# Performance work log

Measured on AMD Instinct MI355X. Metric: run time of the kernel, lower is better.

Reference implementation:

```python
import jax, jax.numpy as jnp
import numpy as np

MARGIN = 0.3
N, D = 8192, 128
NUM_CLASSES = 512


def setup_inputs() -> dict:
    key = jax.random.key(0)
    k1, k2 = jax.random.split(key)
    embeddings = jax.random.normal(k1, (N, D), dtype=jnp.float32)
    targets = jax.random.randint(k2, (N,), 0, NUM_CLASSES, dtype=jnp.int64)
    return {"embeddings": embeddings, "targets": targets}


def reference(embeddings, targets):
    x = embeddings.astype(jnp.float32)
    # pairwise squared-euclidean: ||xi||^2 + ||xj||^2 - 2 xi.xj, clamped then sqrt
    sq = jnp.sum(x * x, axis=1)  # [N]
    dist = sq[:, None] + sq[None, :] - 2.0 * (x @ x.T)
    dist = jnp.sqrt(jnp.clip(dist, 1e-12, None))  # [N, N]

    is_pos = targets[:, None] == targets[None, :]  # includes diagonal, as in torch code

    # batch-hard mining: per-row hardest positive (max) and hardest negative (min)
    dist_ap = jnp.max(jnp.where(is_pos, dist, -jnp.inf), axis=1)
    dist_an = jnp.min(jnp.where(is_pos, jnp.inf, dist), axis=1)

    # MarginRankingLoss(margin)(dist_an, dist_ap, y=1) = mean(relu(margin - (dist_an - dist_ap)))
    loss = jnp.mean(jax.nn.relu(dist_ap - dist_an + MARGIN))
    return loss
```

## Files before the change

kernel.cpp:

```cpp
#include <hip/hip_runtime.h>
#include <hip/hip_bf16.h>

#define N_ROWS 8192
#define DIM 128
#define MARGIN_F 0.3f

typedef __attribute__((ext_vector_type(8))) short short8;
typedef __attribute__((ext_vector_type(4))) float f32x4;
typedef __attribute__((ext_vector_type(4))) int int4v;

__global__ __launch_bounds__(256) void prep_kernel(
    const float* __restrict__ x, const int* __restrict__ tgt,
    unsigned short* __restrict__ xbA, unsigned short* __restrict__ xbB,
    float2* __restrict__ meta, int* __restrict__ apb, int* __restrict__ anb) {
  const int w = threadIdx.x >> 6, l = threadIdx.x & 63;
  const int row = blockIdx.x * 4 + w;
  float2 v = reinterpret_cast<const float2*>(x + (size_t)row * DIM)[l];
  __hip_bfloat16 b0 = __float2bfloat16(v.x);
  __hip_bfloat16 b1 = __float2bfloat16(v.y);
  __hip_bfloat16 a0 = __float2bfloat16(-2.f * v.x);
  __hip_bfloat16 a1 = __float2bfloat16(-2.f * v.y);
  ushort2 stB, stA;
  stB.x = *reinterpret_cast<unsigned short*>(&b0);
  stB.y = *reinterpret_cast<unsigned short*>(&b1);
  stA.x = *reinterpret_cast<unsigned short*>(&a0);
  stA.y = *reinterpret_cast<unsigned short*>(&a1);
  const int c16 = row >> 4, l15r = row & 15;
  const int unit = c16 * 256 + (l >> 4) * 64 + ((l >> 2) & 3) * 16 + l15r;
  reinterpret_cast<ushort2*>(xbB)[unit * 4 + (l & 3)] = stB;
  reinterpret_cast<ushort2*>(xbA)[unit * 4 + (l & 3)] = stA;

  float s = v.x * v.x + v.y * v.y;
  #pragma unroll
  for (int off = 32; off >= 1; off >>= 1) s += __shfl_xor(s, off);
  if (l == 0) {
    float2 m;
    m.x = s;
    m.y = __int_as_float(tgt[row]);
    meta[row] = m;
    apb[row] = 0x00000000;
    anb[row] = 0x7f800000;
  }
}

__global__ __launch_bounds__(256, 2) void gram_mine_kernel(
    const unsigned short* __restrict__ xbA, const unsigned short* __restrict__ xbB,
    const float2* __restrict__ meta, int* __restrict__ apb, int* __restrict__ anb) {
  const int t = threadIdx.x;
  const int w = t >> 6, l = t & 63;
  const int l15 = l & 15, l4 = l >> 4;
  const int rb = blockIdx.x * 128 + w * 32;
  const int chunk = blockIdx.y * 512;
  const int chunkb = chunk >> 4;

  const short8* xfA = reinterpret_cast<const short8*>(xbA);
  const short8* xfB = reinterpret_cast<const short8*>(xbB);

  short8 a0[4], a1[4];
  #pragma unroll
  for (int kk = 0; kk < 4; ++kk) {
    a0[kk] = xfA[(rb >> 4) * 256 + kk * 64 + l];
    a1[kk] = xfA[((rb >> 4) + 1) * 256 + kk * 64 + l];
  }

  int t_r[8];
  #pragma unroll
  for (int rf = 0; rf < 2; ++rf)
    #pragma unroll
    for (int rg = 0; rg < 4; ++rg)
      t_r[rf * 4 + rg] = __float_as_int(meta[rb + rf * 16 + l4 * 4 + rg].y);

  float ap2[8], an2[8];
  #pragma unroll
  for (int i = 0; i < 8; ++i) { ap2[i] = -__builtin_inff(); an2[i] = __builtin_inff(); }

  short8 b0[8], b1[8], b2[8], b3[8];
  float2 m0[2], m1[2], m2[2], m3[2];
  f32x4 accA[2][2], accB[2][2];

#define PREF(IDX, BB, MC) do {                                                \
    const int cb16_ = chunkb + (IDX) * 2;                                     \
    _Pragma("unroll")                                                         \
    for (int kk_ = 0; kk_ < 4; ++kk_) {                                       \
      BB[kk_ * 2 + 0] = xfB[(cb16_ + 0) * 256 + kk_ * 64 + l];                \
      BB[kk_ * 2 + 1] = xfB[(cb16_ + 1) * 256 + kk_ * 64 + l];                \
    }                                                                         \
    MC[0] = meta[chunk + (IDX) * 32 + l15];                                   \
    MC[1] = meta[chunk + (IDX) * 32 + 16 + l15]; } while (0)

#define MFMA_T(BB, MC, ACC) do {                                              \
    _Pragma("unroll")                                                         \
    for (int cf_ = 0; cf_ < 2; ++cf_) {                                       \
      float s_ = MC[cf_].x;                                                   \
      f32x4 ci_ = {s_, s_, s_, s_};                                           \
      ACC[0][cf_] = ci_; ACC[1][cf_] = ci_;                                   \
    }                                                                         \
    __builtin_amdgcn_s_setprio(1);                                            \
    _Pragma("unroll")                                                         \
    for (int kk_ = 0; kk_ < 4; ++kk_) {                                       \
      _Pragma("unroll")                                                       \
      for (int cf_ = 0; cf_ < 2; ++cf_) {                                     \
        ACC[0][cf_] = __builtin_amdgcn_mfma_f32_16x16x32_bf16(                \
            a0[kk_], BB[kk_ * 2 + cf_], ACC[0][cf_], 0, 0, 0);                \
        ACC[1][cf_] = __builtin_amdgcn_mfma_f32_16x16x32_bf16(                \
            a1[kk_], BB[kk_ * 2 + cf_], ACC[1][cf_], 0, 0, 0);                \
      } }                                                                     \
    __builtin_amdgcn_s_setprio(0); } while (0)

#define EPI_T(ACC, MC) do {                                                   \
    _Pragma("unroll")                                                         \
    for (int cf_ = 0; cf_ < 2; ++cf_) {                                       \
      const int tc_ = __float_as_int(MC[cf_].y);                              \
      _Pragma("unroll")                                                       \
      for (int rf_ = 0; rf_ < 2; ++rf_) {                                     \
        _Pragma("unroll")                                                     \
        for (int rg_ = 0; rg_ < 4; ++rg_) {                                   \
          const int ix_ = rf_ * 4 + rg_;                                      \
          float v_ = ACC[rf_][cf_][rg_];                                      \
          bool p_ = (t_r[ix_] == tc_);                                        \
          ap2[ix_] = p_ ? fmaxf(ap2[ix_], v_) : ap2[ix_];                     \
          an2[ix_] = p_ ? an2[ix_] : fminf(an2[ix_], v_);                     \
        } } } } while (0)

  PREF(0, b0, m0);
  PREF(1, b1, m1);
  PREF(2, b2, m2); MFMA_T(b0, m0, accA);
  PREF(3, b3, m3); MFMA_T(b1, m1, accB); EPI_T(accA, m0);

  #pragma unroll 1
  for (int q = 0; q < 3; ++q) {
    const int tb = 4 * q + 2;
    PREF(tb + 2, b0, m0); MFMA_T(b2, m2, accA); EPI_T(accB, m1);
    PREF(tb + 3, b1, m1); MFMA_T(b3, m3, accB); EPI_T(accA, m2);
    PREF(tb + 4, b2, m2); MFMA_T(b0, m0, accA); EPI_T(accB, m3);
    PREF(tb + 5, b3, m3); MFMA_T(b1, m1, accB); EPI_T(accA, m0);
  }
  MFMA_T(b2, m2, accA); EPI_T(accB, m1);
  MFMA_T(b3, m3, accB); EPI_T(accA, m2);
  EPI_T(accB, m3);

#undef PREF
#undef MFMA_T
#undef EPI_T

  #pragma unroll
  for (int i = 0; i < 8; ++i) {
    #pragma unroll
    for (int off = 1; off < 16; off <<= 1) {
      ap2[i] = fmaxf(ap2[i], __shfl_xor(ap2[i], off));
      an2[i] = fminf(an2[i], __shfl_xor(an2[i], off));
    }
  }
  if (l15 == 0) {
    #pragma unroll
    for (int rf = 0; rf < 2; ++rf)
      #pragma unroll
      for (int rg = 0; rg < 4; ++rg) {
        int row = rb + rf * 16 + l4 * 4 + rg;
        float sqr = meta[row].x;
        float a2 = fmaxf(ap2[rf * 4 + rg] + sqr, 1e-12f);
        float n2 = fmaxf(an2[rf * 4 + rg] + sqr, 1e-12f);
        atomicMax(apb + row, __float_as_int(a2));
        atomicMin(anb + row, __float_as_int(n2));
      }
  }
}

__global__ __launch_bounds__(1024) void loss_kernel(
    const int4v* __restrict__ apb, const int4v* __restrict__ anb,
    float* __restrict__ out) {
  __shared__ float red[16];
  float s = 0.f;
  for (int i = threadIdx.x; i < N_ROWS / 4; i += 1024) {
    int4v a4 = apb[i], n4 = anb[i];
    #pragma unroll
    for (int j = 0; j < 4; ++j) {
      float ap = sqrtf(__int_as_float(a4[j]));
      float an = sqrtf(__int_as_float(n4[j]));
      float li = ap - an + MARGIN_F;
      s += li > 0.f ? li : 0.f;
    }
  }
  #pragma unroll
  for (int off = 32; off >= 1; off >>= 1) s += __shfl_xor(s, off);
  const int w = threadIdx.x >> 6, l = threadIdx.x & 63;
  if (l == 0) red[w] = s;
  __syncthreads();
  if (threadIdx.x < 16) {
    float v = red[threadIdx.x];
    #pragma unroll
    for (int off = 8; off >= 1; off >>= 1) v += __shfl_xor(v, off);
    if (threadIdx.x == 0) out[0] = v / (float)N_ROWS;
  }
}

extern "C" void kernel_launch(void* const* d_in, const int* in_sizes, int n_in,
                              void* d_out, int out_size, void* d_ws, size_t ws_size,
                              hipStream_t stream) {
  const float* x = (const float*)d_in[0];
  const int* tgt = (const int*)d_in[1];
  float* out = (float*)d_out;

  char* ws = (char*)d_ws;
  unsigned short* xbA = (unsigned short*)ws;
  unsigned short* xbB = (unsigned short*)(ws + 2097152);
  float2* meta = (float2*)(ws + 4194304);
  int* apb = (int*)(ws + 4194304 + 65536);
  int* anb = (int*)(ws + 4194304 + 65536 + 32768);

  prep_kernel<<<2048, 256, 0, stream>>>(x, tgt, xbA, xbB, meta, apb, anb);
  gram_mine_kernel<<<dim3(64, 16), 256, 0, stream>>>(xbA, xbB, meta, apb, anb);
  loss_kernel<<<1, 1024, 0, stream>>>((const int4v*)apb, (const int4v*)anb, out);
}
```

Measured before the change: 47.90 us.

## Double per-wave row tile to 64 rows and simplify B prefetch to double buffering

Each wave now keeps 64 rows of A fragments in registers instead of 32, so every loaded B column fragment is reused across four MFMA row tiles. This halves the number of row blocks in the grid (32x16) and the total B traffic from global/L2. The four-deep B prefetch ring with separate MFMA/epilogue stages is replaced by a two-buffer ring with the epilogue fused right after the MFMAs. Register pressure rises and the grid shrinks to 512 blocks, which may reduce occupancy and MFMA/epilogue overlap.

```diff
diff --git a/kernel.cpp b/kernel.cpp
--- a/kernel.cpp
+++ b/kernel.cpp
@@ -49,34 +49,33 @@
   const int t = threadIdx.x;
   const int w = t >> 6, l = t & 63;
   const int l15 = l & 15, l4 = l >> 4;
-  const int rb = blockIdx.x * 128 + w * 32;
+  const int rb = blockIdx.x * 256 + w * 64;
   const int chunk = blockIdx.y * 512;
   const int chunkb = chunk >> 4;
 
   const short8* xfA = reinterpret_cast<const short8*>(xbA);
   const short8* xfB = reinterpret_cast<const short8*>(xbB);
 
-  short8 a0[4], a1[4];
-  #pragma unroll
-  for (int kk = 0; kk < 4; ++kk) {
-    a0[kk] = xfA[(rb >> 4) * 256 + kk * 64 + l];
-    a1[kk] = xfA[((rb >> 4) + 1) * 256 + kk * 64 + l];
-  }
-
-  int t_r[8];
-  #pragma unroll
-  for (int rf = 0; rf < 2; ++rf)
+  short8 a[4][4];
+  #pragma unroll
+  for (int rf = 0; rf < 4; ++rf)
+    #pragma unroll
+    for (int kk = 0; kk < 4; ++kk)
+      a[rf][kk] = xfA[((rb >> 4) + rf) * 256 + kk * 64 + l];
+
+  int t_r[16];
+  #pragma unroll
+  for (int rf = 0; rf < 4; ++rf)
     #pragma unroll
     for (int rg = 0; rg < 4; ++rg)
       t_r[rf * 4 + rg] = __float_as_int(meta[rb + rf * 16 + l4 * 4 + rg].y);
 
-  float ap2[8], an2[8];
-  #pragma unroll
-  for (int i = 0; i < 8; ++i) { ap2[i] = -__builtin_inff(); an2[i] = __builtin_inff(); }
-
-  short8 b0[8], b1[8], b2[8], b3[8];
-  float2 m0[2], m1[2], m2[2], m3[2];
-  f32x4 accA[2][2], accB[2][2];
+  float ap2[16], an2[16];
+  #pragma unroll
+  for (int i = 0; i < 16; ++i) { ap2[i] = -__builtin_inff(); an2[i] = __builtin_inff(); }
+
+  short8 b0[8], b1[8];
+  float2 m0[2], m1[2];
 
 #define PREF(IDX, BB, MC) do {                                                \
     const int cb16_ = chunkb + (IDX) * 2;                                     \
@@ -88,63 +87,54 @@
     MC[0] = meta[chunk + (IDX) * 32 + l15];                                   \
     MC[1] = meta[chunk + (IDX) * 32 + 16 + l15]; } while (0)
 
-#define MFMA_T(BB, MC, ACC) do {                                              \
+#define TILE(BB, MC) do {                                                     \
+    f32x4 acc_[4][2];                                                         \
     _Pragma("unroll")                                                         \
     for (int cf_ = 0; cf_ < 2; ++cf_) {                                       \
       float s_ = MC[cf_].x;                                                   \
       f32x4 ci_ = {s_, s_, s_, s_};                                           \
-      ACC[0][cf_] = ci_; ACC[1][cf_] = ci_;                                   \
+      _Pragma("unroll")                                                       \
+      for (int rf_ = 0; rf_ < 4; ++rf_) acc_[rf_][cf_] = ci_;                 \
     }                                                                         \
     __builtin_amdgcn_s_setprio(1);                                            \
     _Pragma("unroll")                                                         \
     for (int kk_ = 0; kk_ < 4; ++kk_) {                                       \
       _Pragma("unroll")                                                       \
       for (int cf_ = 0; cf_ < 2; ++cf_) {                                     \
-        ACC[0][cf_] = __builtin_amdgcn_mfma_f32_16x16x32_bf16(                \
-            a0[kk_], BB[kk_ * 2 + cf_], ACC[0][cf_], 0, 0, 0);                \
-        ACC[1][cf_] = __builtin_amdgcn_mfma_f32_16x16x32_bf16(                \
-            a1[kk_], BB[kk_ * 2 + cf_], ACC[1][cf_], 0, 0, 0);                \
+        _Pragma("unroll")                                                     \
+        for (int rf_ = 0; rf_ < 4; ++rf_)                                     \
+          acc_[rf_][cf_] = __builtin_amdgcn_mfma_f32_16x16x32_bf16(           \
+              a[rf_][kk_], BB[kk_ * 2 + cf_], acc_[rf_][cf_], 0, 0, 0);       \
       } }                                                                     \
-    __builtin_amdgcn_s_setprio(0); } while (0)
-
-#define EPI_T(ACC, MC) do {                                                   \
+    __builtin_amdgcn_s_setprio(0);                                            \
     _Pragma("unroll")                                                         \
     for (int cf_ = 0; cf_ < 2; ++cf_) {                                       \
       const int tc_ = __float_as_int(MC[cf_].y);                              \
       _Pragma("unroll")                                                       \
-      for (int rf_ = 0; rf_ < 2; ++rf_) {                                     \
+      for (int rf_ = 0; rf_ < 4; ++rf_) {                                     \
         _Pragma("unroll")                                                     \
         for (int rg_ = 0; rg_ < 4; ++rg_) {                                   \
           const int ix_ = rf_ * 4 + rg_;                                      \
-          float v_ = ACC[rf_][cf_][rg_];                                      \
+          float v_ = acc_[rf_][cf_][rg_];                                     \
           bool p_ = (t_r[ix_] == tc_);                                        \
           ap2[ix_] = p_ ? fmaxf(ap2[ix_], v_) : ap2[ix_];                     \
           an2[ix_] = p_ ? an2[ix_] : fminf(an2[ix_], v_);                     \
         } } } } while (0)
 
   PREF(0, b0, m0);
-  PREF(1, b1, m1);
-  PREF(2, b2, m2); MFMA_T(b0, m0, accA);
-  PREF(3, b3, m3); MFMA_T(b1, m1, accB); EPI_T(accA, m0);
-
   #pragma unroll 1
-  for (int q = 0; q < 3; ++q) {
-    const int tb = 4 * q + 2;
-    PREF(tb + 2, b0, m0); MFMA_T(b2, m2, accA); EPI_T(accB, m1);
-    PREF(tb + 3, b1, m1); MFMA_T(b3, m3, accB); EPI_T(accA, m2);
-    PREF(tb + 4, b2, m2); MFMA_T(b0, m0, accA); EPI_T(accB, m3);
-    PREF(tb + 5, b3, m3); MFMA_T(b1, m1, accB); EPI_T(accA, m0);
-  }
-  MFMA_T(b2, m2, accA); EPI_T(accB, m1);
-  MFMA_T(b3, m3, accB); EPI_T(accA, m2);
-  EPI_T(accB, m3);
+  for (int q = 0; q < 7; ++q) {
+    PREF(2 * q + 1, b1, m1); TILE(b0, m0);
+    PREF(2 * q + 2, b0, m0); TILE(b1, m1);
+  }
+  PREF(15, b1, m1); TILE(b0, m0);
+  TILE(b1, m1);
 
 #undef PREF
-#undef MFMA_T
-#undef EPI_T
-
-  #pragma unroll
-  for (int i = 0; i < 8; ++i) {
+#undef TILE
+
+  #pragma unroll
+  for (int i = 0; i < 16; ++i) {
     #pragma unroll
     for (int off = 1; off < 16; off <<= 1) {
       ap2[i] = fmaxf(ap2[i], __shfl_xor(ap2[i], off));
@@ -153,7 +143,7 @@
   }
   if (l15 == 0) {
     #pragma unroll
-    for (int rf = 0; rf < 2; ++rf)
+    for (int rf = 0; rf < 4; ++rf)
       #pragma unroll
       for (int rg = 0; rg < 4; ++rg) {
         int row = rb + rf * 16 + l4 * 4 + rg;
@@ -209,6 +199,6 @@
   int* anb = (int*)(ws + 4194304 + 65536 + 32768);
 
   prep_kernel<<<2048, 256, 0, stream>>>(x, tgt, xbA, xbB, meta, apb, anb);
-  gram_mine_kernel<<<dim3(64, 16), 256, 0, stream>>>(xbA, xbB, meta, apb, anb);
+  gram_mine_kernel<<<dim3(32, 16), 256, 0, stream>>>(xbA, xbB, meta, apb, anb);
   loss_kernel<<<1, 1024, 0, stream>>>((const int4v*)apb, (const int4v*)anb, out);
 }
```

Result: faster. 45.29 us (-5.5%).

## Interleave two column streams per block and parallelize loss reduction across blocks

Applied to the files above, without the earlier changes.

The gram/mining kernel now gives each block two 512-column chunks and interleaves their MFMA and epilogue work with a shallower two-buffer prefetch. The grid's y dimension is halved, which cuts the number of atomic row merges. The single-block loss kernel is replaced by eight blocks that combine partial sums through a fixed-point 64-bit atomic and a last-block-done counter. This gives more independent MFMA chains per wave and a more parallel final reduction, at the cost of a different register footprint, fewer blocks, and a quantized loss sum.

```diff
diff --git a/kernel.cpp b/kernel.cpp
--- a/kernel.cpp
+++ b/kernel.cpp
@@ -7,12 +7,13 @@
 
 typedef __attribute__((ext_vector_type(8))) short short8;
 typedef __attribute__((ext_vector_type(4))) float f32x4;
-typedef __attribute__((ext_vector_type(4))) int int4v;
 
 __global__ __launch_bounds__(256) void prep_kernel(
     const float* __restrict__ x, const int* __restrict__ tgt,
     unsigned short* __restrict__ xbA, unsigned short* __restrict__ xbB,
-    float2* __restrict__ meta, int* __restrict__ apb, int* __restrict__ anb) {
+    float2* __restrict__ meta, int* __restrict__ apb, int* __restrict__ anb,
+    unsigned long long* __restrict__ lsum, unsigned int* __restrict__ lcnt) {
+  if (blockIdx.x == 0 && threadIdx.x == 0) { *lsum = 0ull; *lcnt = 0u; }
   const int w = threadIdx.x >> 6, l = threadIdx.x & 63;
   const int row = blockIdx.x * 4 + w;
   float2 v = reinterpret_cast<const float2*>(x + (size_t)row * DIM)[l];
@@ -50,8 +51,8 @@
   const int w = t >> 6, l = t & 63;
   const int l15 = l & 15, l4 = l >> 4;
   const int rb = blockIdx.x * 128 + w * 32;
-  const int chunk = blockIdx.y * 512;
-  const int chunkb = chunk >> 4;
+  const int cu = blockIdx.y * 1024;
+  const int cv = cu + 512;
 
   const short8* xfA = reinterpret_cast<const short8*>(xbA);
   const short8* xfB = reinterpret_cast<const short8*>(xbB);
@@ -74,19 +75,19 @@
   #pragma unroll
   for (int i = 0; i < 8; ++i) { ap2[i] = -__builtin_inff(); an2[i] = __builtin_inff(); }
 
-  short8 b0[8], b1[8], b2[8], b3[8];
-  float2 m0[2], m1[2], m2[2], m3[2];
-  f32x4 accA[2][2], accB[2][2];
-
-#define PREF(IDX, BB, MC) do {                                                \
-    const int cb16_ = chunkb + (IDX) * 2;                                     \
+  short8 bu[8], bv[8];
+  float2 mu0[2], mu1[2], mv0[2], mv1[2];
+  f32x4 accu[2][2], accv[2][2];
+
+#define PREF(BASE, IDX, BB, MC) do {                                          \
+    const int cb16_ = ((BASE) >> 4) + (IDX) * 2;                              \
     _Pragma("unroll")                                                         \
     for (int kk_ = 0; kk_ < 4; ++kk_) {                                       \
       BB[kk_ * 2 + 0] = xfB[(cb16_ + 0) * 256 + kk_ * 64 + l];                \
       BB[kk_ * 2 + 1] = xfB[(cb16_ + 1) * 256 + kk_ * 64 + l];                \
     }                                                                         \
-    MC[0] = meta[chunk + (IDX) * 32 + l15];                                   \
-    MC[1] = meta[chunk + (IDX) * 32 + 16 + l15]; } while (0)
+    MC[0] = meta[(BASE) + (IDX) * 32 + l15];                                  \
+    MC[1] = meta[(BASE) + (IDX) * 32 + 16 + l15]; } while (0)
 
 #define MFMA_T(BB, MC, ACC) do {                                              \
     _Pragma("unroll")                                                         \
@@ -122,22 +123,21 @@
           an2[ix_] = p_ ? an2[ix_] : fminf(an2[ix_], v_);                     \
         } } } } while (0)
 
-  PREF(0, b0, m0);
-  PREF(1, b1, m1);
-  PREF(2, b2, m2); MFMA_T(b0, m0, accA);
-  PREF(3, b3, m3); MFMA_T(b1, m1, accB); EPI_T(accA, m0);
+  PREF(cu, 0, bu, mu0);
+  PREF(cv, 0, bv, mv0);
 
   #pragma unroll 1
-  for (int q = 0; q < 3; ++q) {
-    const int tb = 4 * q + 2;
-    PREF(tb + 2, b0, m0); MFMA_T(b2, m2, accA); EPI_T(accB, m1);
-    PREF(tb + 3, b1, m1); MFMA_T(b3, m3, accB); EPI_T(accA, m2);
-    PREF(tb + 4, b2, m2); MFMA_T(b0, m0, accA); EPI_T(accB, m3);
-    PREF(tb + 5, b3, m3); MFMA_T(b1, m1, accB); EPI_T(accA, m0);
-  }
-  MFMA_T(b2, m2, accA); EPI_T(accB, m1);
-  MFMA_T(b3, m3, accB); EPI_T(accA, m2);
-  EPI_T(accB, m3);
+  for (int q = 0; q < 8; ++q) {
+    const int te = 2 * q;
+    const int n1 = te + 1;
+    const int n2 = (te + 2 < 16) ? te + 2 : 15;
+    MFMA_T(bu, mu0, accu); PREF(cu, n1, bu, mu1);
+    MFMA_T(bv, mv0, accv); PREF(cv, n1, bv, mv1);
+    EPI_T(accu, mu0); EPI_T(accv, mv0);
+    MFMA_T(bu, mu1, accu); PREF(cu, n2, bu, mu0);
+    MFMA_T(bv, mv1, accv); PREF(cv, n2, bv, mv0);
+    EPI_T(accu, mu1); EPI_T(accv, mv1);
+  }
 
 #undef PREF
 #undef MFMA_T
@@ -167,20 +167,15 @@
 }
 
 __global__ __launch_bounds__(1024) void loss_kernel(
-    const int4v* __restrict__ apb, const int4v* __restrict__ anb,
+    const int* __restrict__ apb, const int* __restrict__ anb,
+    unsigned long long* __restrict__ lsum, unsigned int* __restrict__ lcnt,
     float* __restrict__ out) {
   __shared__ float red[16];
-  float s = 0.f;
-  for (int i = threadIdx.x; i < N_ROWS / 4; i += 1024) {
-    int4v a4 = apb[i], n4 = anb[i];
-    #pragma unroll
-    for (int j = 0; j < 4; ++j) {
-      float ap = sqrtf(__int_as_float(a4[j]));
-      float an = sqrtf(__int_as_float(n4[j]));
-      float li = ap - an + MARGIN_F;
-      s += li > 0.f ? li : 0.f;
-    }
-  }
+  const int i = blockIdx.x * 1024 + threadIdx.x;
+  float ap = sqrtf(__int_as_float(apb[i]));
+  float an = sqrtf(__int_as_float(anb[i]));
+  float li = ap - an + MARGIN_F;
+  float s = li > 0.f ? li : 0.f;
   #pragma unroll
   for (int off = 32; off >= 1; off >>= 1) s += __shfl_xor(s, off);
   const int w = threadIdx.x >> 6, l = threadIdx.x & 63;
@@ -190,7 +185,16 @@
     float v = red[threadIdx.x];
     #pragma unroll
     for (int off = 8; off >= 1; off >>= 1) v += __shfl_xor(v, off);
-    if (threadIdx.x == 0) out[0] = v / (float)N_ROWS;
+    if (threadIdx.x == 0) {
+      unsigned long long q = (unsigned long long)(long long)((double)v * 4194304.0);
+      atomicAdd(lsum, q);
+      __threadfence();
+      unsigned int old = atomicAdd(lcnt, 1u);
+      if (old == gridDim.x - 1) {
+        unsigned long long tot = atomicAdd(lsum, 0ull);
+        out[0] = (float)((double)tot * (1.0 / 4194304.0) / (double)N_ROWS);
+      }
+    }
   }
 }
 
@@ -205,10 +209,12 @@
   unsigned short* xbA = (unsigned short*)ws;
   unsigned short* xbB = (unsigned short*)(ws + 2097152);
   float2* meta = (float2*)(ws + 4194304);
-  int* apb = (int*)(ws + 4194304 + 65536);
-  int* anb = (int*)(ws + 4194304 + 65536 + 32768);
-
-  prep_kernel<<<2048, 256, 0, stream>>>(x, tgt, xbA, xbB, meta, apb, anb);
-  gram_mine_kernel<<<dim3(64, 16), 256, 0, stream>>>(xbA, xbB, meta, apb, anb);
-  loss_kernel<<<1, 1024, 0, stream>>>((const int4v*)apb, (const int4v*)anb, out);
-}
+  int* apb = (int*)(ws + 4259840);
+  int* anb = (int*)(ws + 4292608);
+  unsigned long long* lsum = (unsigned long long*)(ws + 4325376);
+  unsigned int* lcnt = (unsigned int*)(ws + 4325384);
+
+  prep_kernel<<<2048, 256, 0, stream>>>(x, tgt, xbA, xbB, meta, apb, anb, lsum, lcnt);
+  gram_mine_kernel<<<dim3(64, 8), 256, 0, stream>>>(xbA, xbB, meta, apb, anb);
+  loss_kernel<<<8, 1024, 0, stream>>>(apb, anb, lsum, lcnt, out);
+}
```

Measured after the change: 47.54 us. About the same (-0.8%).
